# Optimization experiments

Hardware: AMD Instinct MI355X
Metric: run time of the kernel (lower is better)

Reference implementation:

```python
import jax, jax.numpy as jnp
import numpy as np

B, H, W, C = 8, 50, 50, 256
N_ROIS = 256
ROI_SIZE = 28  # >= pool grid so every bin is non-empty


def setup_inputs() -> dict:
    key = jax.random.key(0)
    k1, k2, k3, k4 = jax.random.split(key, 4)
    feat = jax.random.normal(k1, (B, H, W, C), dtype=jnp.float32)
    batch_idx = jax.random.randint(k2, (N_ROIS,), 0, B)
    x1 = jax.random.randint(k3, (N_ROIS,), 0, W - ROI_SIZE + 1)
    y1 = jax.random.randint(k4, (N_ROIS,), 0, H - ROI_SIZE + 1)
    # rois: (image_index, x1, y1, x2, y2), inclusive coordinates
    rois = jnp.stack([batch_idx, x1, y1, x1 + ROI_SIZE - 1, y1 + ROI_SIZE - 1], axis=1).astype(jnp.int32)
    return {"feat": feat, "rois": rois, "pool_height": 7, "pool_width": 7}


def _roi_max_pool(feat, rois, ph, pw):
    n = rois.shape[0]
    h, w = feat.shape[1], feat.shape[2]
    c = feat.shape[3]
    img, x1, y1, x2, y2 = (rois[:, i] for i in range(5))
    roi_h = (y2 - y1 + 1)  # [N]
    roi_w = (x2 - x1 + 1)

    # Per-pixel bin assignment (adaptive partition): bin = floor(offset * pool / extent)
    dy = jnp.arange(h)[None, :] - y1[:, None]                      # [N,H]
    dx = jnp.arange(w)[None, :] - x1[:, None]                      # [N,W]
    row_bin = jnp.minimum(dy * ph // roi_h[:, None], ph - 1)       # [N,H]
    col_bin = jnp.minimum(dx * pw // roi_w[:, None], pw - 1)       # [N,W]
    row_ok = (dy >= 0) & (dy < roi_h[:, None])
    col_ok = (dx >= 0) & (dx < roi_w[:, None])

    valid = row_ok[:, :, None] & col_ok[:, None, :]                # [N,H,W]
    bin_id = row_bin[:, :, None] * pw + col_bin[:, None, :]        # [N,H,W]
    seg = jnp.arange(n)[:, None, None] * (ph * pw) + bin_id
    dump = n * ph * pw  # junk segment for out-of-ROI pixels
    seg = jnp.where(valid, seg, dump)

    feat_n = feat[img]                                             # [N,H,W,C] gather per ROI
    out = jax.ops.segment_max(
        feat_n.reshape(n * h * w, c), seg.reshape(n * h * w),
        num_segments=n * ph * pw + 1,
    )[: n * ph * pw]
    return out.reshape(n, ph, pw, c)                               # [N,ph,pw,C]


def reference(feat, rois, pool_height, pool_width):
    return _roi_max_pool(feat, rois, int(pool_height), int(pool_width))
```

## Files before the change

### kernel.cpp

```cpp
#include <hip/hip_runtime.h>

constexpr int Hf = 50, Wf = 50, Cf = 256;
constexpr int PH = 7, PW = 7;
constexpr int C4 = Cf / 4;

__global__ __launch_bounds__(256) void roipool_kernel(
    const float4* __restrict__ feat,
    const int*    __restrict__ rois,
    float4*       __restrict__ out,
    int n_bins) {
  int bin  = blockIdx.x * 4 + (threadIdx.x >> 6);
  if (bin >= n_bins) return;
  int lane = threadIdx.x & 63;

  int n  = bin / (PH * PW);
  int r  = bin - n * (PH * PW);
  int py = r / PW;
  int px = r - py * PW;

  const int* roi = rois + n * 5;
  int img = roi[0];
  int x1  = roi[1];
  int y1  = roi[2];
  int x2  = roi[3];
  int y2  = roi[4];
  int roi_h = y2 - y1 + 1;
  int roi_w = x2 - x1 + 1;

  int hs = (py * roi_h + PH - 1) / PH;
  int he = ((py + 1) * roi_h + PH - 1) / PH;
  int ws = (px * roi_w + PW - 1) / PW;
  int we = ((px + 1) * roi_w + PW - 1) / PW;

  const float4* fb = feat + (size_t)img * (Hf * Wf * C4) + lane;

  float4 m = make_float4(-INFINITY, -INFINITY, -INFINITY, -INFINITY);

  if (he - hs == 4 && we - ws == 4) {
    const float4* p0 = fb + (size_t)(y1 + hs) * (Wf * C4) + (size_t)(x1 + ws) * C4;
#pragma unroll
    for (int dy = 0; dy < 4; ++dy) {
      const float4* prow = p0 + (size_t)dy * (Wf * C4);
#pragma unroll
      for (int dx = 0; dx < 4; ++dx) {
        float4 v = prow[(size_t)dx * C4];
        m.x = fmaxf(m.x, v.x);
        m.y = fmaxf(m.y, v.y);
        m.z = fmaxf(m.z, v.z);
        m.w = fmaxf(m.w, v.w);
      }
    }
  } else {
    for (int dy = hs; dy < he; ++dy) {
      int y = y1 + dy;
      const float4* prow = fb + (size_t)y * (Wf * C4);
      for (int dx = ws; dx < we; ++dx) {
        int x = x1 + dx;
        float4 v = prow[(size_t)x * C4];
        m.x = fmaxf(m.x, v.x);
        m.y = fmaxf(m.y, v.y);
        m.z = fmaxf(m.z, v.z);
        m.w = fmaxf(m.w, v.w);
      }
    }
  }

  out[(size_t)bin * C4 + lane] = m;
}

extern "C" void kernel_launch(void* const* d_in, const int* in_sizes, int n_in,
                              void* d_out, int out_size, void* d_ws, size_t ws_size,
                              hipStream_t stream) {
  const float* feat = (const float*)d_in[0];
  const int*   rois = (const int*)d_in[1];
  int n_rois = in_sizes[1] / 5;
  int n_bins = n_rois * PH * PW;
  int blocks = (n_bins + 3) / 4;

  roipool_kernel<<<blocks, 256, 0, stream>>>(
      (const float4*)feat, rois, (float4*)d_out, n_bins);
}
```

Baseline: 91.90 us.

## Group ROIs by image and remap blocks per XCD for L2 locality

Adds a single-block counting-sort kernel that orders ROIs by image index into workspace. The pooling kernel then remaps block IDs so each XCD gets a contiguous range of the sorted work, meaning ROIs from the same image are served from the same XCD L2. The aim is to cut redundant HBM/L2 fills of feature maps across the eight XCDs. In exchange it adds an extra serial kernel launch and an indirection load per block.

```diff
diff --git a/kernel.cpp b/kernel.cpp
--- a/kernel.cpp
+++ b/kernel.cpp
@@ -3,20 +3,49 @@
 constexpr int Hf = 50, Wf = 50, Cf = 256;
 constexpr int PH = 7, PW = 7;
 constexpr int C4 = Cf / 4;
+constexpr int NXCD = 8;
+
+__global__ __launch_bounds__(256) void sort_rois_kernel(
+    const int* __restrict__ rois, int n_rois, int n_images,
+    int* __restrict__ order) {
+  __shared__ int cnt[64];
+  __shared__ int base[64];
+  for (int i = threadIdx.x; i < n_images; i += blockDim.x) cnt[i] = 0;
+  __syncthreads();
+  for (int t = threadIdx.x; t < n_rois; t += blockDim.x)
+    atomicAdd(&cnt[rois[t * 5]], 1);
+  __syncthreads();
+  if (threadIdx.x == 0) {
+    int acc = 0;
+    for (int i = 0; i < n_images; ++i) { base[i] = acc; acc += cnt[i]; }
+  }
+  __syncthreads();
+  for (int t = threadIdx.x; t < n_rois; t += blockDim.x) {
+    int slot = atomicAdd(&base[rois[t * 5]], 1);
+    order[slot] = t;
+  }
+}
 
 __global__ __launch_bounds__(256) void roipool_kernel(
     const float4* __restrict__ feat,
     const int*    __restrict__ rois,
+    const int*    __restrict__ order,
     float4*       __restrict__ out,
-    int n_bins) {
-  int bin  = blockIdx.x * 4 + (threadIdx.x >> 6);
-  if (bin >= n_bins) return;
+    int n_bins, int q, int rr) {
+  int i   = blockIdx.x;
+  int xcd = i % NXCD;
+  int w   = (xcd < rr ? xcd * (q + 1) : rr * (q + 1) + (xcd - rr) * q)
+          + i / NXCD;
+
+  int p = w * 4 + (threadIdx.x >> 6);
+  if (p >= n_bins) return;
   int lane = threadIdx.x & 63;
 
-  int n  = bin / (PH * PW);
-  int r  = bin - n * (PH * PW);
-  int py = r / PW;
-  int px = r - py * PW;
+  int s  = p / (PH * PW);
+  int rb = p - s * (PH * PW);
+  int n  = order[s];
+  int py = rb / PW;
+  int px = rb - py * PW;
 
   const int* roi = rois + n * 5;
   int img = roi[0];
@@ -65,7 +94,7 @@
     }
   }
 
-  out[(size_t)bin * C4 + lane] = m;
+  out[((size_t)n * (PH * PW) + rb) * C4 + lane] = m;
 }
 
 extern "C" void kernel_launch(void* const* d_in, const int* in_sizes, int n_in,
@@ -73,10 +102,16 @@
                               hipStream_t stream) {
   const float* feat = (const float*)d_in[0];
   const int*   rois = (const int*)d_in[1];
-  int n_rois = in_sizes[1] / 5;
-  int n_bins = n_rois * PH * PW;
-  int blocks = (n_bins + 3) / 4;
+  int n_rois   = in_sizes[1] / 5;
+  int n_images = in_sizes[0] / (Hf * Wf * Cf);
+  int n_bins   = n_rois * PH * PW;
+  int blocks   = (n_bins + 3) / 4;
+  int q  = blocks / NXCD;
+  int rr = blocks % NXCD;
 
+  int* order = (int*)d_ws;
+
+  sort_rois_kernel<<<1, 256, 0, stream>>>(rois, n_rois, n_images, order);
   roipool_kernel<<<blocks, 256, 0, stream>>>(
-      (const float4*)feat, rois, (float4*)d_out, n_bins);
+      (const float4*)feat, rois, order, (float4*)d_out, n_bins, q, rr);
 }
```

Result: faster. 84.37 us (-8.2%).

## Precompute vertical 4-row max per image, then reduce horizontally per bin

Applied to the files above, without the earlier changes.

Adds a first kernel that computes, for every image position, the max over 4 consecutive rows into a workspace buffer, with an XCD-aware block remapping. The bin kernel then only reads 4 column-max vectors per bin instead of 16 raw pixels when the ROI is exactly 28x28. The cost is an extra full pass over every image plus an extra kernel launch, and the fast path is specialised to the fixed ROI size of the test setup.

```diff
diff --git a/kernel.cpp b/kernel.cpp
--- a/kernel.cpp
+++ b/kernel.cpp
@@ -3,20 +3,54 @@
 constexpr int Hf = 50, Wf = 50, Cf = 256;
 constexpr int PH = 7, PW = 7;
 constexpr int C4 = Cf / 4;
+constexpr int Hc = Hf - 3;
+constexpr int NXCD = 8;
 
-__global__ __launch_bounds__(256) void roipool_kernel(
+__global__ __launch_bounds__(256) void colmax_kernel(
     const float4* __restrict__ feat,
+    float4*       __restrict__ colmax,
+    int n_waves, int q, int rr) {
+  int i   = blockIdx.x;
+  int xcd = i % NXCD;
+  int w   = (xcd < rr ? xcd * (q + 1) : rr * (q + 1) + (xcd - rr) * q)
+          + i / NXCD;
+
+  int wave = w * 4 + (threadIdx.x >> 6);
+  if (wave >= n_waves) return;
+  int lane = threadIdx.x & 63;
+
+  int b  = wave / (Hc * Wf);
+  int r  = wave - b * (Hc * Wf);
+  int y  = r / Wf;
+  int x  = r - y * Wf;
+
+  const float4* p = feat + ((size_t)(b * Hf + y) * Wf + x) * C4 + lane;
+  float4 m = p[0];
+#pragma unroll
+  for (int dy = 1; dy < 4; ++dy) {
+    float4 v = p[(size_t)dy * (Wf * C4)];
+    m.x = fmaxf(m.x, v.x);
+    m.y = fmaxf(m.y, v.y);
+    m.z = fmaxf(m.z, v.z);
+    m.w = fmaxf(m.w, v.w);
+  }
+  colmax[((size_t)(b * Hc + y) * Wf + x) * C4 + lane] = m;
+}
+
+__global__ __launch_bounds__(256) void binmax_kernel(
+    const float4* __restrict__ feat,
+    const float4* __restrict__ colmax,
     const int*    __restrict__ rois,
     float4*       __restrict__ out,
     int n_bins) {
-  int bin  = blockIdx.x * 4 + (threadIdx.x >> 6);
+  int bin = blockIdx.x * 4 + (threadIdx.x >> 6);
   if (bin >= n_bins) return;
   int lane = threadIdx.x & 63;
 
   int n  = bin / (PH * PW);
-  int r  = bin - n * (PH * PW);
-  int py = r / PW;
-  int px = r - py * PW;
+  int rb = bin - n * (PH * PW);
+  int py = rb / PW;
+  int px = rb - py * PW;
 
   const int* roi = rois + n * 5;
   int img = roi[0];
@@ -27,36 +61,30 @@
   int roi_h = y2 - y1 + 1;
   int roi_w = x2 - x1 + 1;
 
-  int hs = (py * roi_h + PH - 1) / PH;
-  int he = ((py + 1) * roi_h + PH - 1) / PH;
-  int ws = (px * roi_w + PW - 1) / PW;
-  int we = ((px + 1) * roi_w + PW - 1) / PW;
-
-  const float4* fb = feat + (size_t)img * (Hf * Wf * C4) + lane;
-
-  float4 m = make_float4(-INFINITY, -INFINITY, -INFINITY, -INFINITY);
-
-  if (he - hs == 4 && we - ws == 4) {
-    const float4* p0 = fb + (size_t)(y1 + hs) * (Wf * C4) + (size_t)(x1 + ws) * C4;
+  float4 m;
+  if (roi_h == 28 && roi_w == 28) {
+    const float4* p = colmax
+        + ((size_t)(img * Hc + (y1 + 4 * py)) * Wf + (x1 + 4 * px)) * C4 + lane;
+    m = p[0];
 #pragma unroll
-    for (int dy = 0; dy < 4; ++dy) {
-      const float4* prow = p0 + (size_t)dy * (Wf * C4);
-#pragma unroll
-      for (int dx = 0; dx < 4; ++dx) {
-        float4 v = prow[(size_t)dx * C4];
-        m.x = fmaxf(m.x, v.x);
-        m.y = fmaxf(m.y, v.y);
-        m.z = fmaxf(m.z, v.z);
-        m.w = fmaxf(m.w, v.w);
-      }
+    for (int dx = 1; dx < 4; ++dx) {
+      float4 v = p[(size_t)dx * C4];
+      m.x = fmaxf(m.x, v.x);
+      m.y = fmaxf(m.y, v.y);
+      m.z = fmaxf(m.z, v.z);
+      m.w = fmaxf(m.w, v.w);
     }
   } else {
+    int hs = (py * roi_h + PH - 1) / PH;
+    int he = ((py + 1) * roi_h + PH - 1) / PH;
+    int ws = (px * roi_w + PW - 1) / PW;
+    int we = ((px + 1) * roi_w + PW - 1) / PW;
+    const float4* fb = feat + (size_t)img * (Hf * Wf * C4) + lane;
+    m = make_float4(-INFINITY, -INFINITY, -INFINITY, -INFINITY);
     for (int dy = hs; dy < he; ++dy) {
-      int y = y1 + dy;
-      const float4* prow = fb + (size_t)y * (Wf * C4);
+      const float4* prow = fb + (size_t)(y1 + dy) * (Wf * C4);
       for (int dx = ws; dx < we; ++dx) {
-        int x = x1 + dx;
-        float4 v = prow[(size_t)x * C4];
+        float4 v = prow[(size_t)(x1 + dx) * C4];
         m.x = fmaxf(m.x, v.x);
         m.y = fmaxf(m.y, v.y);
         m.z = fmaxf(m.z, v.z);
@@ -73,10 +101,20 @@
                               hipStream_t stream) {
   const float* feat = (const float*)d_in[0];
   const int*   rois = (const int*)d_in[1];
-  int n_rois = in_sizes[1] / 5;
-  int n_bins = n_rois * PH * PW;
-  int blocks = (n_bins + 3) / 4;
+  int n_rois   = in_sizes[1] / 5;
+  int n_images = in_sizes[0] / (Hf * Wf * Cf);
+  int n_bins   = n_rois * PH * PW;
 
-  roipool_kernel<<<blocks, 256, 0, stream>>>(
-      (const float4*)feat, rois, (float4*)d_out, n_bins);
+  float4* colmax = (float4*)d_ws;
+
+  int waves_a  = n_images * Hc * Wf;
+  int blocks_a = (waves_a + 3) / 4;
+  int qa  = blocks_a / NXCD;
+  int ra  = blocks_a % NXCD;
+  colmax_kernel<<<blocks_a, 256, 0, stream>>>(
+      (const float4*)feat, colmax, waves_a, qa, ra);
+
+  int blocks_c = (n_bins + 3) / 4;
+  binmax_kernel<<<blocks_c, 256, 0, stream>>>(
+      (const float4*)feat, colmax, rois, (float4*)d_out, n_bins);
 }
```

Measured after the change: 86.62 us. -5.7%, faster.
